# Kernel tuning notes

Measured on AMD Instinct MI355X. Metric: run time of the kernel, lower is better.

Reference implementation:

```python
import jax, jax.numpy as jnp
import numpy as np

N_NODES = 50000


def setup_inputs() -> dict:
    key = jax.random.key(0)
    k1, k2, k3 = jax.random.split(key, 3)
    x = jax.random.normal(k1, (N_NODES, 256), dtype=jnp.float32)
    edge_index = jax.random.randint(k2, (2, 1600000), 0, N_NODES, dtype=jnp.int64)
    W = jax.random.normal(k3, (256, 256), dtype=jnp.float32) / np.sqrt(256.0)
    b = jnp.zeros((256,), dtype=jnp.float32)
    return {"x": x, "edge_index": edge_index, "W": W, "b": b}


def reference(x, edge_index, W, b):
    # PyG GCNConv: add self-loops, symmetric normalization, linear, aggregate, bias; then ReLU.
    n = x.shape[0]
    self_loops = jnp.arange(n, dtype=edge_index.dtype)
    src = jnp.concatenate([edge_index[0], self_loops])  # [E+N]
    dst = jnp.concatenate([edge_index[1], self_loops])  # [E+N]

    # degree from incoming edges (incl. self loops)
    deg = jax.ops.segment_sum(jnp.ones_like(dst, dtype=x.dtype), dst, num_segments=n)
    dinv = jnp.where(deg > 0, jax.lax.rsqrt(deg), 0.0)
    norm = dinv[src] * dinv[dst]  # [E+N]

    xw = x @ W  # [N, out] linear first (GCNConv transforms then propagates)
    msgs = xw[src] * norm[:, None]  # gather + edge-normalize
    agg = jax.ops.segment_sum(msgs, dst, num_segments=n)  # scatter-add
    return jax.nn.relu(agg + b)
```

## Files before the change

kernel.cpp:

```cpp
#include <hip/hip_runtime.h>
#include <hip/hip_bf16.h>


#define FEATS 256
#define MAXBUCK 200
#define P1_CAP 64
#define BCAP 10240

typedef __bf16 bf16x8 __attribute__((ext_vector_type(8)));
typedef float f32x4 __attribute__((ext_vector_type(4)));

__device__ __forceinline__ unsigned short f2bf(float f) {
  unsigned u = __float_as_uint(f);
  u += 0x7fffu + ((u >> 16) & 1u);
  return (unsigned short)(u >> 16);
}
__device__ __forceinline__ float bflo(unsigned u) { return __uint_as_float(u << 16); }
__device__ __forceinline__ float bfhi(unsigned u) { return __uint_as_float(u & 0xFFFF0000u); }


__global__ __launch_bounds__(256) void zero_i32(int* __restrict__ p, int n) {
  int i = blockIdx.x * 256 + threadIdx.x;
  if (i < n) p[i] = 0;
}

__global__ __launch_bounds__(256) void pass1_bin(const int* __restrict__ src,
                                                 const int* __restrict__ dst,
                                                 int E, int nbuck,
                                                 int* __restrict__ gcursor,
                                                 unsigned* __restrict__ temp) {
  __shared__ unsigned lbuf[MAXBUCK * P1_CAP];
  __shared__ int lcnt[MAXBUCK];
  __shared__ int lbase[MAXBUCK];
  const int tid = threadIdx.x;
  for (int i = tid; i < nbuck; i += 256) lcnt[i] = 0;
  __syncthreads();

  const int e0 = blockIdx.x * 4096;
  #pragma unroll
  for (int i = 0; i < 16; ++i) {
    int e = e0 + i * 256 + tid;
    if (e < E) {
      unsigned d = (unsigned)dst[e];
      unsigned p = (d << 16) | (unsigned)src[e];
      int b = (int)(d >> 8);
      int pos = atomicAdd(&lcnt[b], 1);
      if (pos < P1_CAP) {
        lbuf[b * P1_CAP + pos] = p;
      } else {
        int gp = atomicAdd(&gcursor[b], 1);
        temp[(size_t)b * BCAP + gp] = p;
      }
    }
  }
  __syncthreads();
  if (tid < nbuck) {
    int c = lcnt[tid]; if (c > P1_CAP) c = P1_CAP;
    lcnt[tid] = c;
    lbase[tid] = atomicAdd(&gcursor[tid], c);
  }
  __syncthreads();
  for (int i = tid; i < nbuck * P1_CAP; i += 256) {
    int b = i >> 6, j = i & (P1_CAP - 1);
    if (j < lcnt[b]) temp[(size_t)b * BCAP + lbase[b] + j] = lbuf[i];
  }
}

__global__ __launch_bounds__(256) void scan_buckets(const int* __restrict__ gcursor,
                                                    int* __restrict__ bbase,
                                                    int* __restrict__ row_ptr,
                                                    int nbuck, int n) {
  __shared__ int tmp[256];
  int t = threadIdx.x;
  int v = (t < nbuck) ? min(gcursor[t], BCAP) : 0;
  tmp[t] = v;
  __syncthreads();
  #pragma unroll
  for (int off = 1; off < 256; off <<= 1) {
    int x = (t >= off) ? tmp[t - off] : 0;
    __syncthreads();
    tmp[t] += x;
    __syncthreads();
  }
  if (t < nbuck) bbase[t] = tmp[t] - v;
  if (t == 0) row_ptr[n] = tmp[255];
}

__global__ __launch_bounds__(256) void pass2_csr(const unsigned* __restrict__ temp,
                                                 const int* __restrict__ gcursor,
                                                 const int* __restrict__ bbase,
                                                 unsigned short* __restrict__ csr16,
                                                 int* __restrict__ row_ptr,
                                                 float* __restrict__ dinv, int n) {
  __shared__ unsigned ebuf[BCAP];
  __shared__ unsigned short sorted[BCAP];
  __shared__ int hist[256], scn[256], sexcl[256], ofs[256];
  const int b = blockIdx.x;
  const int tid = threadIdx.x;
  int cnt = gcursor[b]; if (cnt > BCAP) cnt = BCAP;
  const int base = bbase[b];
  const unsigned* tp = temp + (size_t)b * BCAP;

  hist[tid] = 0;
  ofs[tid] = 0;
  for (int i = tid; i < cnt; i += 256) ebuf[i] = tp[i];
  __syncthreads();
  for (int i = tid; i < cnt; i += 256) atomicAdd(&hist[(ebuf[i] >> 16) & 255], 1);
  __syncthreads();

  int v = hist[tid];
  scn[tid] = v;
  __syncthreads();
  #pragma unroll
  for (int off = 1; off < 256; off <<= 1) {
    int x = (tid >= off) ? scn[tid - off] : 0;
    __syncthreads();
    scn[tid] += x;
    __syncthreads();
  }
  int excl = scn[tid] - v;
  sexcl[tid] = excl;
  int node = (b << 8) + tid;
  if (node < n) {
    row_ptr[node] = base + excl;
    dinv[node] = rsqrtf((float)(v + 1));
  }
  __syncthreads();

  for (int i = tid; i < cnt; i += 256) {
    unsigned e = ebuf[i];
    int dl = (int)((e >> 16) & 255);
    int pos = sexcl[dl] + atomicAdd(&ofs[dl], 1);
    sorted[pos] = (unsigned short)(e & 0xFFFFu);
  }
  __syncthreads();
  for (int i = tid; i < cnt; i += 256) csr16[base + i] = sorted[i];
}


__global__ __launch_bounds__(256) void wt_build(const float* __restrict__ W,
                                                unsigned short* __restrict__ Wt) {
  int k = blockIdx.x;
  int nn = threadIdx.x;
  Wt[nn * FEATS + k] = f2bf(W[k * FEATS + nn]);
}


__global__ __launch_bounds__(256) void gemm_mfma(const float* __restrict__ x,
                                                 const unsigned short* __restrict__ Wt,
                                                 const float* __restrict__ dinv,
                                                 unsigned short* __restrict__ xwp, int M) {
  const int wave = (int)((blockIdx.x * 256 + threadIdx.x) >> 6);
  const int lane = (int)(threadIdx.x & 63);
  const int m0 = wave * 16;
  if (m0 >= M) return;
  const int lm = lane & 15;
  const int quad = lane >> 4;

  int arow = m0 + lm; if (arow >= M) arow = M - 1;
  const float* xrow = x + (size_t)arow * FEATS + quad * 8;
  bf16x8 Afrag[8];
  #pragma unroll
  for (int kc = 0; kc < 8; ++kc) {
    const float4 f0 = *(const float4*)(xrow + kc * 32);
    const float4 f1 = *(const float4*)(xrow + kc * 32 + 4);
    union { bf16x8 v; unsigned short u[8]; } a;
    a.u[0] = f2bf(f0.x); a.u[1] = f2bf(f0.y); a.u[2] = f2bf(f0.z); a.u[3] = f2bf(f0.w);
    a.u[4] = f2bf(f1.x); a.u[5] = f2bf(f1.y); a.u[6] = f2bf(f1.z); a.u[7] = f2bf(f1.w);
    Afrag[kc] = a.v;
  }

  float dsc[4];
  #pragma unroll
  for (int r = 0; r < 4; ++r) {
    int rr = m0 + quad * 4 + r; if (rr >= M) rr = M - 1;
    dsc[r] = dinv[rr];
  }

  for (int ct = 0; ct < 16; ++ct) {
    const int c0 = ct * 16;
    const unsigned short* wrow = Wt + (size_t)(c0 + lm) * FEATS + quad * 8;
    f32x4 acc = {0.f, 0.f, 0.f, 0.f};
    #pragma unroll
    for (int kc = 0; kc < 8; ++kc) {
      bf16x8 B = *(const bf16x8*)(wrow + kc * 32);
      acc = __builtin_amdgcn_mfma_f32_16x16x32_bf16(Afrag[kc], B, acc, 0, 0, 0);
    }
    #pragma unroll
    for (int r = 0; r < 4; ++r) {
      int row = m0 + quad * 4 + r;
      if (row < M) xwp[(size_t)row * FEATS + c0 + lm] = f2bf(acc[r] * dsc[r]);
    }
  }
}


__global__ __launch_bounds__(256) void aggregate(const unsigned short* __restrict__ xwp,
                                                 const float* __restrict__ dinv,
                                                 const int* __restrict__ row_ptr,
                                                 const unsigned short* __restrict__ csr16,
                                                 const float* __restrict__ bias,
                                                 float* __restrict__ out, int n) {
  const int node = (int)((blockIdx.x * blockDim.x + threadIdx.x) >> 6);
  const int lane = (int)(threadIdx.x & 63);
  if (node >= n) return;
  const int co = lane << 2;

  uint2 sv = *(const uint2*)(xwp + (((size_t)node) << 8) + co);
  float4 acc;
  acc.x = bflo(sv.x); acc.y = bfhi(sv.x); acc.z = bflo(sv.y); acc.w = bfhi(sv.y);

  const int beg = row_ptr[node];
  const int end = row_ptr[node + 1];
  for (int base = beg; base < end; base += 64) {
    int idx = base + lane;
    int s = (idx < end) ? (int)csr16[idx] : 0;
    int m = end - base;
    if (m > 64) m = 64;
    int i = 0;
    for (; i + 8 <= m; i += 8) {
      uint2 v[8];
      #pragma unroll
      for (int j = 0; j < 8; ++j) {
        int sj = __shfl(s, i + j);
        v[j] = *(const uint2*)(xwp + (((size_t)sj) << 8) + co);
      }
      #pragma unroll
      for (int j = 0; j < 8; ++j) {
        acc.x += bflo(v[j].x); acc.y += bfhi(v[j].x);
        acc.z += bflo(v[j].y); acc.w += bfhi(v[j].y);
      }
    }
    for (; i < m; ++i) {
      int sj = __shfl(s, i);
      uint2 v = *(const uint2*)(xwp + (((size_t)sj) << 8) + co);
      acc.x += bflo(v.x); acc.y += bfhi(v.x);
      acc.z += bflo(v.y); acc.w += bfhi(v.y);
    }
  }

  const float dd = dinv[node];
  const float4 bb = *(const float4*)(bias + co);
  float4 o;
  o.x = fmaxf(fmaf(acc.x, dd, bb.x), 0.f);
  o.y = fmaxf(fmaf(acc.y, dd, bb.y), 0.f);
  o.z = fmaxf(fmaf(acc.z, dd, bb.z), 0.f);
  o.w = fmaxf(fmaf(acc.w, dd, bb.w), 0.f);
  *(float4*)(out + (((size_t)node) << 8) + co) = o;
}


extern "C" void kernel_launch(void* const* d_in, const int* in_sizes, int n_in,
                              void* d_out, int out_size, void* d_ws, size_t ws_size,
                              hipStream_t stream) {
  const float* x  = (const float*)d_in[0];
  const int*   ei = (const int*)d_in[1];
  const float* W  = (const float*)d_in[2];
  const float* b  = (const float*)d_in[3];

  const int n = in_sizes[0] / FEATS;
  const int E = in_sizes[1] / 2;
  const int* src = ei;
  const int* dst = ei + E;
  const int nbuck = (n + 255) >> 8;

  char* ws = (char*)d_ws;
  unsigned short* xwp   = (unsigned short*)(ws);
  unsigned short* Wt    = (unsigned short*)(ws + 25600000);
  float*          dinv  = (float*)(ws + 25731072);
  int*            row_ptr = (int*)(ws + 25931072);
  unsigned short* csr16 = (unsigned short*)(ws + 26131136);
  int*            gcursor = (int*)(ws + 29331136);
  int*            bbase   = (int*)(ws + 29332160);
  unsigned*       temp    = (unsigned*)(ws + 29333184);

  hipLaunchKernelGGL(zero_i32, dim3(1), dim3(256), 0, stream, gcursor, nbuck);
  hipLaunchKernelGGL(wt_build, dim3(256), dim3(256), 0, stream, W, Wt);

  const int g_p1 = (E + 4095) / 4096;
  hipLaunchKernelGGL(pass1_bin, dim3(g_p1), dim3(256), 0, stream, src, dst, E, nbuck, gcursor, temp);
  hipLaunchKernelGGL(scan_buckets, dim3(1), dim3(256), 0, stream, gcursor, bbase, row_ptr, nbuck, n);
  hipLaunchKernelGGL(pass2_csr, dim3(nbuck), dim3(256), 0, stream, temp, gcursor, bbase,
                     csr16, row_ptr, dinv, n);

  const int strips = (n + 15) / 16;
  hipLaunchKernelGGL(gemm_mfma, dim3((strips + 3) / 4), dim3(256), 0, stream, x, Wt, dinv, xwp, n);

  const int g_agg = (n * 64 + 255) / 256;
  hipLaunchKernelGGL(aggregate, dim3(g_agg), dim3(256), 0, stream,
                     xwp, dinv, row_ptr, csr16, b, (float*)d_out, n);
}
```

Baseline: 304.9 us.

## Widen CSR build blocks and split aggregation into column slices across waves

pass1_bin and pass2_csr now run with 1024-thread blocks, so each block has more concurrent workers for binning and the per-bucket sort. The aggregate kernel is restructured so each block handles one of 8 column slices of 32 features for 4 nodes. Each wave processes 8 edges in parallel, with 8 lanes per edge each loading 8 bytes, and then reduces across lane groups with xor shuffles. Nontemporal loads and stores are added for row_ptr, the CSR indices and the output. The slice split raises the number of gathers in flight per wave, but it makes eight times as many blocks re-read row_ptr and the index list, and it adds a cross-lane reduction.

```diff
diff --git a/kernel.cpp b/kernel.cpp
--- a/kernel.cpp
+++ b/kernel.cpp
@@ -24,22 +24,22 @@
   if (i < n) p[i] = 0;
 }
 
-__global__ __launch_bounds__(256) void pass1_bin(const int* __restrict__ src,
-                                                 const int* __restrict__ dst,
-                                                 int E, int nbuck,
-                                                 int* __restrict__ gcursor,
-                                                 unsigned* __restrict__ temp) {
+__global__ __launch_bounds__(1024) void pass1_bin(const int* __restrict__ src,
+                                                  const int* __restrict__ dst,
+                                                  int E, int nbuck,
+                                                  int* __restrict__ gcursor,
+                                                  unsigned* __restrict__ temp) {
   __shared__ unsigned lbuf[MAXBUCK * P1_CAP];
   __shared__ int lcnt[MAXBUCK];
   __shared__ int lbase[MAXBUCK];
   const int tid = threadIdx.x;
-  for (int i = tid; i < nbuck; i += 256) lcnt[i] = 0;
+  for (int i = tid; i < nbuck; i += 1024) lcnt[i] = 0;
   __syncthreads();
 
   const int e0 = blockIdx.x * 4096;
   #pragma unroll
-  for (int i = 0; i < 16; ++i) {
-    int e = e0 + i * 256 + tid;
+  for (int i = 0; i < 4; ++i) {
+    int e = e0 + i * 1024 + tid;
     if (e < E) {
       unsigned d = (unsigned)dst[e];
       unsigned p = (d << 16) | (unsigned)src[e];
@@ -60,7 +60,7 @@
     lbase[tid] = atomicAdd(&gcursor[tid], c);
   }
   __syncthreads();
-  for (int i = tid; i < nbuck * P1_CAP; i += 256) {
+  for (int i = tid; i < nbuck * P1_CAP; i += 1024) {
     int b = i >> 6, j = i & (P1_CAP - 1);
     if (j < lcnt[b]) temp[(size_t)b * BCAP + lbase[b] + j] = lbuf[i];
   }
@@ -86,12 +86,12 @@
   if (t == 0) row_ptr[n] = tmp[255];
 }
 
-__global__ __launch_bounds__(256) void pass2_csr(const unsigned* __restrict__ temp,
-                                                 const int* __restrict__ gcursor,
-                                                 const int* __restrict__ bbase,
-                                                 unsigned short* __restrict__ csr16,
-                                                 int* __restrict__ row_ptr,
-                                                 float* __restrict__ dinv, int n) {
+__global__ __launch_bounds__(1024) void pass2_csr(const unsigned* __restrict__ temp,
+                                                  const int* __restrict__ gcursor,
+                                                  const int* __restrict__ bbase,
+                                                  unsigned short* __restrict__ csr16,
+                                                  int* __restrict__ row_ptr,
+                                                  float* __restrict__ dinv, int n) {
   __shared__ unsigned ebuf[BCAP];
   __shared__ unsigned short sorted[BCAP];
   __shared__ int hist[256], scn[256], sexcl[256], ofs[256];
@@ -101,40 +101,42 @@
   const int base = bbase[b];
   const unsigned* tp = temp + (size_t)b * BCAP;
 
-  hist[tid] = 0;
-  ofs[tid] = 0;
-  for (int i = tid; i < cnt; i += 256) ebuf[i] = tp[i];
-  __syncthreads();
-  for (int i = tid; i < cnt; i += 256) atomicAdd(&hist[(ebuf[i] >> 16) & 255], 1);
-  __syncthreads();
-
-  int v = hist[tid];
-  scn[tid] = v;
+  if (tid < 256) { hist[tid] = 0; ofs[tid] = 0; }
+  for (int i = tid; i < cnt; i += 1024) ebuf[i] = tp[i];
+  __syncthreads();
+  for (int i = tid; i < cnt; i += 1024) atomicAdd(&hist[(ebuf[i] >> 16) & 255], 1);
+  __syncthreads();
+
+  if (tid < 256) scn[tid] = hist[tid];
   __syncthreads();
   #pragma unroll
   for (int off = 1; off < 256; off <<= 1) {
-    int x = (tid >= off) ? scn[tid - off] : 0;
-    __syncthreads();
-    scn[tid] += x;
-    __syncthreads();
-  }
-  int excl = scn[tid] - v;
-  sexcl[tid] = excl;
-  int node = (b << 8) + tid;
-  if (node < n) {
-    row_ptr[node] = base + excl;
-    dinv[node] = rsqrtf((float)(v + 1));
-  }
-  __syncthreads();
-
-  for (int i = tid; i < cnt; i += 256) {
+    int x = 0;
+    if (tid < 256 && tid >= off) x = scn[tid - off];
+    __syncthreads();
+    if (tid < 256) scn[tid] += x;
+    __syncthreads();
+  }
+  if (tid < 256) {
+    int v = hist[tid];
+    int excl = scn[tid] - v;
+    sexcl[tid] = excl;
+    int node = (b << 8) + tid;
+    if (node < n) {
+      row_ptr[node] = base + excl;
+      dinv[node] = rsqrtf((float)(v + 1));
+    }
+  }
+  __syncthreads();
+
+  for (int i = tid; i < cnt; i += 1024) {
     unsigned e = ebuf[i];
     int dl = (int)((e >> 16) & 255);
     int pos = sexcl[dl] + atomicAdd(&ofs[dl], 1);
     sorted[pos] = (unsigned short)(e & 0xFFFFu);
   }
   __syncthreads();
-  for (int i = tid; i < cnt; i += 256) csr16[base + i] = sorted[i];
+  for (int i = tid; i < cnt; i += 1024) csr16[base + i] = sorted[i];
 }
 
 
@@ -201,52 +203,53 @@
                                                  const unsigned short* __restrict__ csr16,
                                                  const float* __restrict__ bias,
                                                  float* __restrict__ out, int n) {
-  const int node = (int)((blockIdx.x * blockDim.x + threadIdx.x) >> 6);
+  const int slice = (int)(blockIdx.x & 7);
+  const int node = (int)((blockIdx.x >> 3) * 4 + (threadIdx.x >> 6));
+  if (node >= n) return;
   const int lane = (int)(threadIdx.x & 63);
-  if (node >= n) return;
-  const int co = lane << 2;
-
-  uint2 sv = *(const uint2*)(xwp + (((size_t)node) << 8) + co);
-  float4 acc;
-  acc.x = bflo(sv.x); acc.y = bfhi(sv.x); acc.z = bflo(sv.y); acc.w = bfhi(sv.y);
-
-  const int beg = row_ptr[node];
-  const int end = row_ptr[node + 1];
-  for (int base = beg; base < end; base += 64) {
-    int idx = base + lane;
-    int s = (idx < end) ? (int)csr16[idx] : 0;
-    int m = end - base;
-    if (m > 64) m = 64;
-    int i = 0;
-    for (; i + 8 <= m; i += 8) {
-      uint2 v[8];
-      #pragma unroll
-      for (int j = 0; j < 8; ++j) {
-        int sj = __shfl(s, i + j);
-        v[j] = *(const uint2*)(xwp + (((size_t)sj) << 8) + co);
-      }
-      #pragma unroll
-      for (int j = 0; j < 8; ++j) {
-        acc.x += bflo(v[j].x); acc.y += bfhi(v[j].x);
-        acc.z += bflo(v[j].y); acc.w += bfhi(v[j].y);
-      }
-    }
-    for (; i < m; ++i) {
-      int sj = __shfl(s, i);
-      uint2 v = *(const uint2*)(xwp + (((size_t)sj) << 8) + co);
-      acc.x += bflo(v.x); acc.y += bfhi(v.x);
-      acc.z += bflo(v.y); acc.w += bfhi(v.y);
-    }
-  }
-
-  const float dd = dinv[node];
-  const float4 bb = *(const float4*)(bias + co);
-  float4 o;
-  o.x = fmaxf(fmaf(acc.x, dd, bb.x), 0.f);
-  o.y = fmaxf(fmaf(acc.y, dd, bb.y), 0.f);
-  o.z = fmaxf(fmaf(acc.z, dd, bb.z), 0.f);
-  o.w = fmaxf(fmaf(acc.w, dd, bb.w), 0.f);
-  *(float4*)(out + (((size_t)node) << 8) + co) = o;
+  const int eg = lane >> 3;
+  const int cl = lane & 7;
+  const int colofs = slice * 32 + cl * 4;
+
+  float a0 = 0.f, a1 = 0.f, a2 = 0.f, a3 = 0.f;
+
+  const int beg = __builtin_nontemporal_load(row_ptr + node);
+  const int end = __builtin_nontemporal_load(row_ptr + node + 1);
+  for (int base = beg; base < end; base += 16) {
+    int i0 = base + eg;
+    int i1 = i0 + 8;
+    if (i0 < end) {
+      int s0 = (int)__builtin_nontemporal_load(csr16 + i0);
+      uint2 v = *(const uint2*)(xwp + (((size_t)s0) << 8) + colofs);
+      a0 += bflo(v.x); a1 += bfhi(v.x); a2 += bflo(v.y); a3 += bfhi(v.y);
+    }
+    if (i1 < end) {
+      int s1 = (int)__builtin_nontemporal_load(csr16 + i1);
+      uint2 v = *(const uint2*)(xwp + (((size_t)s1) << 8) + colofs);
+      a0 += bflo(v.x); a1 += bfhi(v.x); a2 += bflo(v.y); a3 += bfhi(v.y);
+    }
+  }
+
+  #pragma unroll
+  for (int m = 8; m < 64; m <<= 1) {
+    a0 += __shfl_xor(a0, m);
+    a1 += __shfl_xor(a1, m);
+    a2 += __shfl_xor(a2, m);
+    a3 += __shfl_xor(a3, m);
+  }
+
+  if (eg == 0) {
+    uint2 sv = *(const uint2*)(xwp + (((size_t)node) << 8) + colofs);
+    a0 += bflo(sv.x); a1 += bfhi(sv.x); a2 += bflo(sv.y); a3 += bfhi(sv.y);
+    const float dd = dinv[node];
+    const float* bp = bias + colofs;
+    f32x4 o;
+    o.x = fmaxf(fmaf(a0, dd, bp[0]), 0.f);
+    o.y = fmaxf(fmaf(a1, dd, bp[1]), 0.f);
+    o.z = fmaxf(fmaf(a2, dd, bp[2]), 0.f);
+    o.w = fmaxf(fmaf(a3, dd, bp[3]), 0.f);
+    __builtin_nontemporal_store(o, (f32x4*)(out + (((size_t)node) << 8) + colofs));
+  }
 }
 
 
@@ -278,15 +281,15 @@
   hipLaunchKernelGGL(wt_build, dim3(256), dim3(256), 0, stream, W, Wt);
 
   const int g_p1 = (E + 4095) / 4096;
-  hipLaunchKernelGGL(pass1_bin, dim3(g_p1), dim3(256), 0, stream, src, dst, E, nbuck, gcursor, temp);
+  hipLaunchKernelGGL(pass1_bin, dim3(g_p1), dim3(1024), 0, stream, src, dst, E, nbuck, gcursor, temp);
   hipLaunchKernelGGL(scan_buckets, dim3(1), dim3(256), 0, stream, gcursor, bbase, row_ptr, nbuck, n);
-  hipLaunchKernelGGL(pass2_csr, dim3(nbuck), dim3(256), 0, stream, temp, gcursor, bbase,
+  hipLaunchKernelGGL(pass2_csr, dim3(nbuck), dim3(1024), 0, stream, temp, gcursor, bbase,
                      csr16, row_ptr, dinv, n);
 
   const int strips = (n + 15) / 16;
   hipLaunchKernelGGL(gemm_mfma, dim3((strips + 3) / 4), dim3(256), 0, stream, x, Wt, dinv, xwp, n);
 
-  const int g_agg = (n * 64 + 255) / 256;
+  const int g_agg = ((n + 3) / 4) * 8;
   hipLaunchKernelGGL(aggregate, dim3(g_agg), dim3(256), 0, stream,
                      xwp, dinv, row_ptr, csr16, b, (float*)d_out, n);
 }
```

Result: slower. 474.9 us (+55.8%).
